# Performance work log

Hardware: AMD Instinct MI355X
Metric: run time of the kernel (lower is better)

Reference implementation:

```python
import jax, jax.numpy as jnp
import numpy as np

NOPEN = 64
NNIN = 16
NUM_OUTPUT = 64
NLAYER = 4
H = 0.1
TF = 1.0
N_NODES = 50000
N_EDGES = 1600000


def setup_inputs() -> dict:
    key = jax.random.key(0)
    k1, k2, k3, k4, k5, k6 = jax.random.split(key, 6)
    xn = jax.random.normal(k1, (1, NNIN, N_NODES), dtype=jnp.float32)
    iInd = jax.random.randint(k2, (N_EDGES,), 0, N_NODES)
    jInd = jax.random.randint(k3, (N_EDGES,), 0, N_NODES)
    # learned parameters per original init
    K1Nopen = jax.random.normal(k4, (NOPEN, NNIN), dtype=jnp.float32) * 0.01
    KN1 = jnp.eye(NOPEN, dtype=jnp.float32) + jax.random.uniform(k5, (NOPEN, NOPEN), dtype=jnp.float32) * 0.001
    KNclose = jax.random.normal(k6, (NUM_OUTPUT, NOPEN), dtype=jnp.float32) * 0.01
    return {"xn": xn, "iInd": iInd, "jInd": jInd, "n_nodes": N_NODES,
            "K1Nopen": K1Nopen, "KN1": KN1, "KNclose": KNclose}


def _gcn_norm(I, J, n_nodes, dtype):
    # add self-loops, symmetric normalization deg^{-1/2}[row]*deg^{-1/2}[col]
    loops = jnp.arange(n_nodes, dtype=I.dtype)
    I2 = jnp.concatenate([I, loops])
    J2 = jnp.concatenate([J, loops])
    ew = jnp.ones(I2.shape[0], dtype=dtype)
    deg = jax.ops.segment_sum(ew, J2, num_segments=n_nodes)
    dinv = jnp.where(deg > 0, 1.0 / jnp.sqrt(deg), 0.0)
    w = dinv[I2] * dinv[J2]
    return I2, J2, w


def reference(xn, iInd, jInd, n_nodes, K1Nopen, KN1, KNclose):
    I, J, w = _gcn_norm(iInd, jInd, n_nodes, xn.dtype)  # [E+N]

    # OpenFlatLayer: 1x1 conv1d with K1Nopen + relu (openclose=True, norm=False)
    x = jax.nn.relu(jnp.einsum('oi,bin->bon', K1Nopen, xn))  # [1, nopen, N]

    dt = TF / NLAYER
    wb = w[None, None, :]
    for _ in range(NLAYER):
        # nodeGrad: edge features [1, nopen, E]
        g = wb * (x[:, :, I] - x[:, :, J])
        # singleLayer (openclose=False): conv(K), relu, conv(K.t())
        z = jax.nn.relu(jnp.einsum('oi,bie->boe', KN1, g))
        z = jnp.einsum('io,bie->boe', KN1, z)
        # edgeDiv: scatter-add w*z at I minus at J
        wz = jnp.moveaxis(wb * z, -1, 0)  # [E, 1, nopen]
        div = (jax.ops.segment_sum(wz, I, num_segments=n_nodes)
               - jax.ops.segment_sum(wz, J, num_segments=n_nodes))
        div = jnp.moveaxis(div, 0, -1)  # [1, nopen, N]
        # forward Euler: step layer returns -h*div, integrated with dt
        x = x - dt * H * div

    # CloseLayer: 1x1 conv1d, squeeze().t(), log_softmax over channels
    xc = jnp.einsum('oi,bin->bon', KNclose, x)[0].T  # [N, num_output]
    return jax.nn.log_softmax(xc, axis=1)
```

## Files before the change

kernel.cpp:

```cpp
#include <hip/hip_runtime.h>

#define NN 50000
#define NE 1600000
#define C 64
#define NIN 16
#define DTH 0.025f
#define ASC 16.0f
#define USC 64.0f
#define SDIV 16384.0f
#define SLOT 128

#define NB2 256
#define NPB 196
#define CAP 16384
#define ABLK 1024
#define EPB 1563
#define RND 2048
#define BINC 32
#define GSTR 16

typedef _Float16 f16x2 __attribute__((ext_vector_type(2)));
typedef float f32x2 __attribute__((ext_vector_type(2)));
union U32H2 { uint32_t u; f16x2 h; };

#define RL(x, l) __int_as_float(__builtin_amdgcn_readlane(__float_as_int(x), (l)))

__global__ void k_setup(const float* __restrict__ KN1, const float* __restrict__ KNc,
                        float* __restrict__ M2s, float* __restrict__ KMs,
                        int* __restrict__ gcur) {
    if (threadIdx.x < NB2) gcur[threadIdx.x * GSTR] = 0;
    for (int idx = threadIdx.x; idx < C * C; idx += blockDim.x) {
        int p = idx >> 6, o = idx & 63;
        float s1 = 0.f, s2 = 0.f;
        for (int i = 0; i < C; i++) {
            s1 = fmaf(KN1[o * C + i], KN1[p * C + i], s1);
            s2 = fmaf(KNc[o * C + i], KN1[p * C + i], s2);
        }
        M2s[idx] = s1;
        KMs[idx] = s2;
    }
}

static __device__ __forceinline__ void store_u8(uint32_t* __restrict__ u8, int n, int lane, float su) {
    float v1 = __shfl_down(su, 1, 64);
    float v2 = __shfl_down(su, 2, 64);
    float v3 = __shfl_down(su, 3, 64);
    if ((lane & 3) == 0) {
        int p0 = __builtin_amdgcn_cvt_pk_fp8_f32(su, v1, 0, false);
        int p1 = __builtin_amdgcn_cvt_pk_fp8_f32(v2, v3, p0, true);
        u8[n * 16 + (lane >> 2)] = (uint32_t)p1;
    }
}

__launch_bounds__(512)
__global__ void k_binA_open(const int* __restrict__ iInd, const int* __restrict__ jInd,
                            int* __restrict__ gcur, uint32_t* __restrict__ stg,
                            const float* __restrict__ xn, const float* __restrict__ K1,
                            const float* __restrict__ KN1, const float* __restrict__ KNc,
                            _Float16* __restrict__ u0, uint32_t* __restrict__ u8,
                            float* __restrict__ co) {
    __shared__ __align__(16) char smem[36864];
    __shared__ int bcnt[NB2];
    __shared__ int gbase[NB2];
    __shared__ float sxn[NIN][17];
    uint32_t (*bins)[BINC] = (uint32_t(*)[BINC])smem;
    int tid = threadIdx.x;
    int eBeg = blockIdx.x * EPB;
    int eEnd = eBeg + EPB; if (eEnd > NE) eEnd = NE;
    for (int rb = eBeg; rb < eEnd; rb += RND) {
        for (int b = tid; b < NB2; b += 512) bcnt[b] = 0;
        __syncthreads();
        int rEnd = rb + RND; if (rEnd > eEnd) rEnd = eEnd;
        for (int e = rb + tid; e < rEnd; e += 512) {
            int i = __builtin_nontemporal_load(&iInd[e]);
            int j = __builtin_nontemporal_load(&jInd[e]);
            {
                int b = (unsigned)i / NPB;
                uint32_t ent = ((unsigned)(i - b * NPB) << 17) | (unsigned)j;
                int pos = atomicAdd(&bcnt[b], 1);
                if (pos < BINC) bins[b][pos] = ent;
                else { int gp = atomicAdd(&gcur[b * GSTR], 1);
                       if (gp < CAP) stg[(size_t)b * CAP + gp] = ent; }
            }
            {
                int b = (unsigned)j / NPB;
                uint32_t ent = ((unsigned)(j - b * NPB) << 17) | 0x10000u | (unsigned)i;
                int pos = atomicAdd(&bcnt[b], 1);
                if (pos < BINC) bins[b][pos] = ent;
                else { int gp = atomicAdd(&gcur[b * GSTR], 1);
                       if (gp < CAP) stg[(size_t)b * CAP + gp] = ent; }
            }
        }
        __syncthreads();
        if (tid < NB2) {
            int c = bcnt[tid]; if (c > BINC) c = BINC;
            gbase[tid] = (c > 0) ? atomicAdd(&gcur[tid * GSTR], c) : 0;
        }
        __syncthreads();
        for (int idx = tid; idx < NB2 * BINC; idx += 512) {
            int b = idx >> 5, k = idx & (BINC - 1);
            int c = bcnt[b]; if (c > BINC) c = BINC;
            if (k < c) {
                int pos = gbase[b] + k;
                if (pos < CAP) stg[(size_t)b * CAP + pos] = bins[b][k];
            }
        }
        __syncthreads();
    }
    float* sK1 = (float*)smem;
    float* sU  = sK1 + NIN * C;
    float* sC  = sU + C * C;
    for (int idx = tid; idx < NIN * C; idx += 512) {
        int i = idx >> 6, o = idx & 63;
        sK1[idx] = K1[o * NIN + i];
    }
    for (int idx = tid; idx < C * C; idx += 512) {
        int o = idx >> 6, p = idx & 63;
        int sw = (o << 6) | (p ^ ((o & 7) << 2));
        sU[sw] = KN1[idx];
        sC[sw] = KNc[idx];
    }
    int wv = tid >> 6, lane = tid & 63;
    int mb = lane << 6, lx = (lane & 7) << 2;
    int w2 = wv * 2;
    int nit = 3 + (blockIdx.x < 53 ? 1 : 0);
    int fi = tid >> 4, ft = tid & 15;
    float vpre = 0.f;
    if (tid < 256) vpre = xn[fi * NN + blockIdx.x * 16 + ft];
    for (int it = 0; it < nit; it++) {
        __syncthreads();
        if (tid < 256) sxn[fi][ft] = vpre;
        __syncthreads();
        if (it + 1 < nit && tid < 256)
            vpre = xn[fi * NN + blockIdx.x * 16 + (it + 1) * 16384 + ft];
        int pr = blockIdx.x * 8 + wv + it * 8192;
        int nA = pr * 2, nB = nA + 1;
        float xA = 0.f, xB = 0.f;
#pragma unroll
        for (int i = 0; i < NIN; i++) {
            float k1 = sK1[i * C + lane];
            xA = fmaf(k1, sxn[i][w2], xA);
            xB = fmaf(k1, sxn[i][w2 + 1], xB);
        }
        xA = fmaxf(xA, 0.f); xB = fmaxf(xB, 0.f);
        float uA0 = 0.f, uA1 = 0.f, uB0 = 0.f, uB1 = 0.f;
        float cA0 = 0.f, cA1 = 0.f, cB0 = 0.f, cB1 = 0.f;
#pragma unroll
        for (int p0 = 0; p0 < C; p0 += 4) {
            const float4 mu = *(const float4*)&sU[mb + (p0 ^ lx)];
            const float4 mc = *(const float4*)&sC[mb + (p0 ^ lx)];
            float a0 = RL(xA, p0 + 0), a1 = RL(xA, p0 + 1);
            float a2 = RL(xA, p0 + 2), a3 = RL(xA, p0 + 3);
            float b0 = RL(xB, p0 + 0), b1 = RL(xB, p0 + 1);
            float b2 = RL(xB, p0 + 2), b3 = RL(xB, p0 + 3);
            uA0 = fmaf(mu.x, a0, uA0); uA1 = fmaf(mu.y, a1, uA1);
            uA0 = fmaf(mu.z, a2, uA0); uA1 = fmaf(mu.w, a3, uA1);
            uB0 = fmaf(mu.x, b0, uB0); uB1 = fmaf(mu.y, b1, uB1);
            uB0 = fmaf(mu.z, b2, uB0); uB1 = fmaf(mu.w, b3, uB1);
            cA0 = fmaf(mc.x, a0, cA0); cA1 = fmaf(mc.y, a1, cA1);
            cA0 = fmaf(mc.z, a2, cA0); cA1 = fmaf(mc.w, a3, cA1);
            cB0 = fmaf(mc.x, b0, cB0); cB1 = fmaf(mc.y, b1, cB1);
            cB0 = fmaf(mc.z, b2, cB0); cB1 = fmaf(mc.w, b3, cB1);
        }
        float uA = uA0 + uA1, uB = uB0 + uB1;
        u0[(size_t)nA * C + lane] = (_Float16)uA;
        u0[(size_t)nB * C + lane] = (_Float16)uB;
        store_u8(u8, nA, lane, uA * USC);
        store_u8(u8, nB, lane, uB * USC);
        co[(size_t)nA * C + lane] = cA0 + cA1;
        co[(size_t)nB * C + lane] = cB0 + cB1;
    }
}

#define LADJ (NPB * SLOT)
__launch_bounds__(1024)
__global__ void k_binB(const int* __restrict__ gcur, const uint32_t* __restrict__ stg,
                       unsigned* __restrict__ pk, float* __restrict__ dinv,
                       uint32_t* __restrict__ adjp) {
    __shared__ unsigned lcnt[NPB];
    __shared__ uint32_t ladj[LADJ];
    int b = blockIdx.x, tid = threadIdx.x;
    if (tid < NPB) lcnt[tid] = 0;
    __syncthreads();
    int cnt = gcur[b * GSTR]; if (cnt > CAP) cnt = CAP;
    int n0 = b * NPB;
    for (int k = tid; k < cnt; k += 1024) {
        uint32_t ent = stg[(size_t)b * CAP + k];
        int tl = (int)(ent >> 17);
        unsigned sign = (ent >> 16) & 1u;
        unsigned other = ent & 0xFFFFu;
        unsigned ret = atomicAdd(&lcnt[tl], 1u + (sign << 16));
        unsigned slot = ret & 0xFFFFu;
        if (slot < SLOT) ladj[(tl << 7) + slot] = other | (sign << 31);
    }
    __syncthreads();
    if (tid < NPB) {
        int n = n0 + tid;
        if (n < NN) {
            unsigned v = lcnt[tid];
            unsigned c = v & 0xFFFFu; if (c > SLOT) c = SLOT;
            unsigned deg = (v >> 16) + 1u;
            pk[n] = (deg << 16) | c;
            dinv[n] = 1.0f / sqrtf((float)deg);
        }
    }
    int nval = NN - n0; if (nval > NPB) nval = NPB; if (nval < 0) nval = 0;
    int totv = (nval << 7) >> 2;
    uint4* gdst = (uint4*)(adjp + ((size_t)n0 << 7));
    const uint4* lsrc = (const uint4*)ladj;
    for (int v = tid; v < totv; v += 1024) gdst[v] = lsrc[v];
}

__global__ void k_weight(const unsigned* __restrict__ pk, const float* __restrict__ dinv,
                         uint32_t* __restrict__ adjp) {
    int idx = blockIdx.x * 256 + threadIdx.x;
    int n = idx >> 7, p = idx & (SLOT - 1);
    int cnt = (int)(pk[n] & 0xFFFFu); if (cnt > SLOT) cnt = SLOT;
    int pad = (cnt + 31) & ~31;
    if (p < cnt) {
        uint32_t e = adjp[idx];
        int other = (int)(e & 0xFFFFu);
        float a = ASC * dinv[n] * dinv[other];
        float w = 0.5f * a * a;
        if (e >> 31) w = -w;
        U32H2 t; t.u = (unsigned)other; t.h.y = (_Float16)w;
        adjp[idx] = t.u;
    } else if (p < pad) {
        adjp[idx] = 0u;
    }
}

#define ACCR(WW, QQ, A0, A1, A2, A3, U0, U1, U2, U3) {                        \
    U32H2 aw; aw.u = (WW);                                                    \
    float w_ = (float)aw.h.y;                                                 \
    f32x2 lo_ = __builtin_amdgcn_cvt_pk_f32_fp8((int)(QQ), false);            \
    f32x2 hi_ = __builtin_amdgcn_cvt_pk_f32_fp8((int)(QQ), true);             \
    float d0_ = (U0) - lo_.x, d1_ = (U1) - lo_.y;                             \
    float d2_ = (U2) - hi_.x, d3_ = (U3) - hi_.y;                             \
    A0 = fmaf(w_, __builtin_fabsf(d0_), fmaf(__builtin_fabsf(w_), d0_, A0));  \
    A1 = fmaf(w_, __builtin_fabsf(d1_), fmaf(__builtin_fabsf(w_), d1_, A1));  \
    A2 = fmaf(w_, __builtin_fabsf(d2_), fmaf(__builtin_fabsf(w_), d2_, A2));  \
    A3 = fmaf(w_, __builtin_fabsf(d3_), fmaf(__builtin_fabsf(w_), d3_, A3));  \
}

#define GATHER2_BODY(PKA, ADJP, U8R)                                          \
    uint32_t unqA = (U8R)[nA * 16 + li];                                      \
    uint32_t unqB = (U8R)[nB * 16 + li];                                      \
    f32x2 alo = __builtin_amdgcn_cvt_pk_f32_fp8((int)unqA, false);            \
    f32x2 ahi = __builtin_amdgcn_cvt_pk_f32_fp8((int)unqA, true);             \
    f32x2 blo = __builtin_amdgcn_cvt_pk_f32_fp8((int)unqB, false);            \
    f32x2 bhi = __builtin_amdgcn_cvt_pk_f32_fp8((int)unqB, true);             \
    float uA0 = alo.x, uA1 = alo.y, uA2 = ahi.x, uA3 = ahi.y;                 \
    float uB0 = blo.x, uB1 = blo.y, uB2 = bhi.x, uB3 = bhi.y;                 \
    uint2 pk2_ = *(const uint2*)&(PKA)[nA];                                   \
    int degA = (int)(pk2_.x & 0xFFFFu); if (degA > SLOT) degA = SLOT;         \
    int degB = (int)(pk2_.y & 0xFFFFu); if (degB > SLOT) degB = SLOT;         \
    int padA = (degA + 31) & ~31, padB = (degB + 31) & ~31;                   \
    int baseA = nA << 7, baseB = nB << 7;                                     \
    int maxPad = padA > padB ? padA : padB;                                   \
    float aA0 = 0.f, aA1 = 0.f, aA2 = 0.f, aA3 = 0.f;                         \
    float aB0 = 0.f, aB1 = 0.f, aB2 = 0.f, aB3 = 0.f;                         \
    for (int c0 = 0; c0 < maxPad; c0 += 32) {                                 \
        uint32_t wA[8], qA[8], wB[8], qB[8];                                  \
        bool dA = c0 < padA, dB = c0 < padB;                                  \
        if (dA) {                                                             \
            _Pragma("unroll")                                                 \
            for (int r = 0; r < 8; r++) wA[r] = (ADJP)[baseA + c0 + r * 4 + g]; \
        }                                                                     \
        if (dB) {                                                             \
            _Pragma("unroll")                                                 \
            for (int r = 0; r < 8; r++) wB[r] = (ADJP)[baseB + c0 + r * 4 + g]; \
        }                                                                     \
        if (dA) {                                                             \
            _Pragma("unroll")                                                 \
            for (int r = 0; r < 8; r++) qA[r] = (U8R)[(wA[r] & 0xFFFFu) * 16 + li]; \
        }                                                                     \
        if (dB) {                                                             \
            _Pragma("unroll")                                                 \
            for (int r = 0; r < 8; r++) qB[r] = (U8R)[(wB[r] & 0xFFFFu) * 16 + li]; \
        }                                                                     \
        if (dA) {                                                             \
            _Pragma("unroll")                                                 \
            for (int r = 0; r < 8; r++) ACCR(wA[r], qA[r], aA0, aA1, aA2, aA3, uA0, uA1, uA2, uA3) \
        }                                                                     \
        if (dB) {                                                             \
            _Pragma("unroll")                                                 \
            for (int r = 0; r < 8; r++) ACCR(wB[r], qB[r], aB0, aB1, aB2, aB3, uB0, uB1, uB2, uB3) \
        }                                                                     \
    }                                                                         \
    aA0 += __shfl_xor(aA0, 16, 64); aA0 += __shfl_xor(aA0, 32, 64);           \
    aA1 += __shfl_xor(aA1, 16, 64); aA1 += __shfl_xor(aA1, 32, 64);           \
    aA2 += __shfl_xor(aA2, 16, 64); aA2 += __shfl_xor(aA2, 32, 64);           \
    aA3 += __shfl_xor(aA3, 16, 64); aA3 += __shfl_xor(aA3, 32, 64);           \
    aB0 += __shfl_xor(aB0, 16, 64); aB0 += __shfl_xor(aB0, 32, 64);           \
    aB1 += __shfl_xor(aB1, 16, 64); aB1 += __shfl_xor(aB1, 32, 64);           \
    aB2 += __shfl_xor(aB2, 16, 64); aB2 += __shfl_xor(aB2, 32, 64);           \
    aB3 += __shfl_xor(aB3, 16, 64); aB3 += __shfl_xor(aB3, 32, 64);           \
    float rA0 = __shfl(aA0, lane >> 2, 64), rA1 = __shfl(aA1, lane >> 2, 64); \
    float rA2 = __shfl(aA2, lane >> 2, 64), rA3 = __shfl(aA3, lane >> 2, 64); \
    float rB0 = __shfl(aB0, lane >> 2, 64), rB1 = __shfl(aB1, lane >> 2, 64); \
    float rB2 = __shfl(aB2, lane >> 2, 64), rB3 = __shfl(aB3, lane >> 2, 64); \
    float sA_lane = (lane & 2) ? ((lane & 1) ? rA3 : rA2)                     \
                               : ((lane & 1) ? rA1 : rA0);                    \
    float sB_lane = (lane & 2) ? ((lane & 1) ? rB3 : rB2)                     \
                               : ((lane & 1) ? rB1 : rB0);

#define STAGE_MT(SMT, SRC) {                                                  \
    for (int idx = threadIdx.x; idx < C * C; idx += 256) {                    \
        int p_ = idx >> 6, c_ = idx & 63;                                     \
        (SMT)[(c_ << 6) | (p_ ^ ((c_ & 7) << 2))] = (SRC)[idx];               \
    }                                                                         \
}

#define MATVEC2(SMT, SAV, SBV, DUA, DUB) {                                    \
    float mA0_ = 0.f, mA1_ = 0.f, mB0_ = 0.f, mB1_ = 0.f;                     \
    int mb_ = (lane << 6), lx_ = (lane & 7) << 2;                             \
    _Pragma("unroll")                                                         \
    for (int p0 = 0; p0 < 64; p0 += 4) {                                      \
        const float4 mv = *(const float4*)&(SMT)[mb_ + (p0 ^ lx_)];           \
        mA0_ = fmaf(mv.x, RL(SAV, p0 + 0), mA0_);                             \
        mA1_ = fmaf(mv.y, RL(SAV, p0 + 1), mA1_);                             \
        mA0_ = fmaf(mv.z, RL(SAV, p0 + 2), mA0_);                             \
        mA1_ = fmaf(mv.w, RL(SAV, p0 + 3), mA1_);                             \
        mB0_ = fmaf(mv.x, RL(SBV, p0 + 0), mB0_);                             \
        mB1_ = fmaf(mv.y, RL(SBV, p0 + 1), mB1_);                             \
        mB0_ = fmaf(mv.z, RL(SBV, p0 + 2), mB0_);                             \
        mB1_ = fmaf(mv.w, RL(SBV, p0 + 3), mB1_);                             \
    }                                                                         \
    DUA = mA0_ + mA1_; DUB = mB0_ + mB1_;                                     \
}

__launch_bounds__(256, 8)
__global__ void k_gather_upd(const unsigned* __restrict__ pk, const uint32_t* __restrict__ adjp,
                             const uint32_t* __restrict__ u8r, const _Float16* __restrict__ ucur,
                             const float* __restrict__ M2s, float* __restrict__ sacc,
                             _Float16* __restrict__ unext, uint32_t* __restrict__ u8w, int beta) {
    __shared__ float sMt[C * C];
    STAGE_MT(sMt, M2s)
    __syncthreads();
    int wv = threadIdx.x >> 6, lane = threadIdx.x & 63;
    int g = lane >> 4, li = lane & 15;
    int nA = (blockIdx.x * 4 + wv) * 2;
    int nB = nA + 1;
    GATHER2_BODY(pk, adjp, u8r)
    float duA, duB;
    MATVEC2(sMt, sA_lane, sB_lane, duA, duB)
    float unewA = (float)ucur[(size_t)nA * C + lane] - (DTH / SDIV) * duA;
    float unewB = (float)ucur[(size_t)nB * C + lane] - (DTH / SDIV) * duB;
    unext[(size_t)nA * C + lane] = (_Float16)unewA;
    unext[(size_t)nB * C + lane] = (_Float16)unewB;
    store_u8(u8w, nA, lane, unewA * USC);
    store_u8(u8w, nB, lane, unewB * USC);
    size_t ixA = (size_t)nA * C + lane, ixB = (size_t)nB * C + lane;
    sacc[ixA] = beta ? (sacc[ixA] + sA_lane) : sA_lane;
    sacc[ixB] = beta ? (sacc[ixB] + sB_lane) : sB_lane;
}

__launch_bounds__(256, 8)
__global__ void k_gather_close(const unsigned* __restrict__ pk, const uint32_t* __restrict__ adjp,
                               const uint32_t* __restrict__ u8r, const float* __restrict__ KMs,
                               const float* __restrict__ sacc, const float* __restrict__ co,
                               float* __restrict__ out) {
    __shared__ float sKMt[C * C];
    STAGE_MT(sKMt, KMs)
    __syncthreads();
    int wv = threadIdx.x >> 6, lane = threadIdx.x & 63;
    int g = lane >> 4, li = lane & 15;
    int nA = (blockIdx.x * 4 + wv) * 2;
    int nB = nA + 1;
    GATHER2_BODY(pk, adjp, u8r)
    float stotA = sA_lane + sacc[(size_t)nA * C + lane];
    float stotB = sB_lane + sacc[(size_t)nB * C + lane];
    float dxA, dxB;
    MATVEC2(sKMt, stotA, stotB, dxA, dxB)
    float oA = co[(size_t)nA * C + lane] - (DTH / SDIV) * dxA;
    float oB = co[(size_t)nB * C + lane] - (DTH / SDIV) * dxB;
    float mA = oA, mB = oB;
#pragma unroll
    for (int off2 = 32; off2; off2 >>= 1) {
        mA = fmaxf(mA, __shfl_xor(mA, off2, 64));
        mB = fmaxf(mB, __shfl_xor(mB, off2, 64));
    }
    float sumA = expf(oA - mA), sumB = expf(oB - mB);
#pragma unroll
    for (int off2 = 32; off2; off2 >>= 1) {
        sumA += __shfl_xor(sumA, off2, 64);
        sumB += __shfl_xor(sumB, off2, 64);
    }
    out[(size_t)nA * C + lane] = oA - mA - logf(sumA);
    out[(size_t)nB * C + lane] = oB - mB - logf(sumB);
}

extern "C" void kernel_launch(void* const* d_in, const int* in_sizes, int n_in,
                              void* d_out, int out_size, void* d_ws, size_t ws_size,
                              hipStream_t stream) {
    (void)in_sizes; (void)n_in; (void)out_size; (void)ws_size;
    const float* xn   = (const float*)d_in[0];
    const int* iInd   = (const int*)d_in[1];
    const int* jInd   = (const int*)d_in[2];
    const float* K1   = (const float*)d_in[4];
    const float* KN1  = (const float*)d_in[5];
    const float* KNc  = (const float*)d_in[6];
    float* out = (float*)d_out;

    char* base = (char*)d_ws;
    size_t off = 0;
    auto alloc = [&](size_t bytes) { char* p = base + off; off = (off + bytes + 255) & ~(size_t)255; return p; };
    float* M2s  = (float*)alloc(C * C * 4);
    float* KMs  = (float*)alloc(C * C * 4);
    int* gcur   = (int*)alloc(NB2 * GSTR * 4);
    unsigned* pk = (unsigned*)alloc(NN * 4);
    float* dinv = (float*)alloc(NN * 4);
    float* co   = (float*)alloc((size_t)NN * C * 4);
    float* sacc = (float*)alloc((size_t)NN * C * 4);
    _Float16* ua = (_Float16*)alloc((size_t)NN * C * 2);
    _Float16* ub = (_Float16*)alloc((size_t)NN * C * 2);
    uint32_t* u8a = (uint32_t*)alloc((size_t)NN * 16 * 4);
    uint32_t* u8b = (uint32_t*)alloc((size_t)NN * 16 * 4);
    uint32_t* stg = (uint32_t*)alloc((size_t)NB2 * CAP * 4);
    uint32_t* adjp = (uint32_t*)alloc((size_t)NN * SLOT * 4);

    k_setup<<<1, 256, 0, stream>>>(KN1, KNc, M2s, KMs, gcur);
    k_binA_open<<<ABLK, 512, 0, stream>>>(iInd, jInd, gcur, stg, xn, K1, KN1, KNc, ua, u8a, co);
    k_binB<<<NB2, 1024, 0, stream>>>(gcur, stg, pk, dinv, adjp);
    k_weight<<<(NN * SLOT) / 256, 256, 0, stream>>>(pk, dinv, adjp);

    const int GB = NN / 8;
    k_gather_upd<<<GB, 256, 0, stream>>>(pk, adjp, u8a, ua, M2s, sacc, ub, u8b, 0);
    k_gather_upd<<<GB, 256, 0, stream>>>(pk, adjp, u8b, ub, M2s, sacc, ua, u8a, 1);
    k_gather_upd<<<GB, 256, 0, stream>>>(pk, adjp, u8a, ua, M2s, sacc, ub, u8b, 1);
    k_gather_close<<<GB, 256, 0, stream>>>(pk, adjp, u8b, KMs, sacc, co, out);
}
```

Before: 459.6 us.

## Prefetch next adjacency chunk, pack accumulation math, store raw edge weight

```diff
diff --git a/kernel.cpp b/kernel.cpp
--- a/kernel.cpp
+++ b/kernel.cpp
@@ -221,73 +221,91 @@
         uint32_t e = adjp[idx];
         int other = (int)(e & 0xFFFFu);
         float a = ASC * dinv[n] * dinv[other];
-        float w = 0.5f * a * a;
-        if (e >> 31) w = -w;
-        U32H2 t; t.u = (unsigned)other; t.h.y = (_Float16)w;
+        if (e >> 31) a = -a;
+        U32H2 t; t.u = (unsigned)other; t.h.y = (_Float16)a;
         adjp[idx] = t.u;
     } else if (p < pad) {
         adjp[idx] = 0u;
     }
 }
 
-#define ACCR(WW, QQ, A0, A1, A2, A3, U0, U1, U2, U3) {                        \
+#define ACCR(WW, QQ, A01, A23, U01, U23) {                                    \
     U32H2 aw; aw.u = (WW);                                                    \
-    float w_ = (float)aw.h.y;                                                 \
+    float a_ = (float)aw.h.y;                                                 \
+    f32x2 av_; av_.x = a_; av_.y = a_;                                        \
     f32x2 lo_ = __builtin_amdgcn_cvt_pk_f32_fp8((int)(QQ), false);            \
     f32x2 hi_ = __builtin_amdgcn_cvt_pk_f32_fp8((int)(QQ), true);             \
-    float d0_ = (U0) - lo_.x, d1_ = (U1) - lo_.y;                             \
-    float d2_ = (U2) - hi_.x, d3_ = (U3) - hi_.y;                             \
-    A0 = fmaf(w_, __builtin_fabsf(d0_), fmaf(__builtin_fabsf(w_), d0_, A0));  \
-    A1 = fmaf(w_, __builtin_fabsf(d1_), fmaf(__builtin_fabsf(w_), d1_, A1));  \
-    A2 = fmaf(w_, __builtin_fabsf(d2_), fmaf(__builtin_fabsf(w_), d2_, A2));  \
-    A3 = fmaf(w_, __builtin_fabsf(d3_), fmaf(__builtin_fabsf(w_), d3_, A3));  \
+    f32x2 t01_ = av_ * ((U01) - lo_);                                         \
+    f32x2 t23_ = av_ * ((U23) - hi_);                                         \
+    t01_ = __builtin_elementwise_max(t01_, zz);                               \
+    t23_ = __builtin_elementwise_max(t23_, zz);                               \
+    A01 = av_ * t01_ + A01;                                                   \
+    A23 = av_ * t23_ + A23;                                                   \
 }
 
 #define GATHER2_BODY(PKA, ADJP, U8R)                                          \
     uint32_t unqA = (U8R)[nA * 16 + li];                                      \
     uint32_t unqB = (U8R)[nB * 16 + li];                                      \
-    f32x2 alo = __builtin_amdgcn_cvt_pk_f32_fp8((int)unqA, false);            \
-    f32x2 ahi = __builtin_amdgcn_cvt_pk_f32_fp8((int)unqA, true);             \
-    f32x2 blo = __builtin_amdgcn_cvt_pk_f32_fp8((int)unqB, false);            \
-    f32x2 bhi = __builtin_amdgcn_cvt_pk_f32_fp8((int)unqB, true);             \
-    float uA0 = alo.x, uA1 = alo.y, uA2 = ahi.x, uA3 = ahi.y;                 \
-    float uB0 = blo.x, uB1 = blo.y, uB2 = bhi.x, uB3 = bhi.y;                 \
+    f32x2 uA01 = __builtin_amdgcn_cvt_pk_f32_fp8((int)unqA, false);           \
+    f32x2 uA23 = __builtin_amdgcn_cvt_pk_f32_fp8((int)unqA, true);            \
+    f32x2 uB01 = __builtin_amdgcn_cvt_pk_f32_fp8((int)unqB, false);           \
+    f32x2 uB23 = __builtin_amdgcn_cvt_pk_f32_fp8((int)unqB, true);            \
     uint2 pk2_ = *(const uint2*)&(PKA)[nA];                                   \
     int degA = (int)(pk2_.x & 0xFFFFu); if (degA > SLOT) degA = SLOT;         \
     int degB = (int)(pk2_.y & 0xFFFFu); if (degB > SLOT) degB = SLOT;         \
     int padA = (degA + 31) & ~31, padB = (degB + 31) & ~31;                   \
     int baseA = nA << 7, baseB = nB << 7;                                     \
     int maxPad = padA > padB ? padA : padB;                                   \
-    float aA0 = 0.f, aA1 = 0.f, aA2 = 0.f, aA3 = 0.f;                         \
-    float aB0 = 0.f, aB1 = 0.f, aB2 = 0.f, aB3 = 0.f;                         \
+    f32x2 zz; zz.x = 0.f; zz.y = 0.f;                                         \
+    f32x2 aA01 = zz, aA23 = zz, aB01 = zz, aB23 = zz;                         \
+    uint32_t wA[8], wB[8];                                                    \
+    if (padA > 0) {                                                           \
+        _Pragma("unroll")                                                     \
+        for (int r = 0; r < 8; r++) wA[r] = (ADJP)[baseA + r * 4 + g];        \
+    }                                                                         \
+    if (padB > 0) {                                                           \
+        _Pragma("unroll")                                                     \
+        for (int r = 0; r < 8; r++) wB[r] = (ADJP)[baseB + r * 4 + g];        \
+    }                                                                         \
     for (int c0 = 0; c0 < maxPad; c0 += 32) {                                 \
-        uint32_t wA[8], qA[8], wB[8], qB[8];                                  \
+        uint32_t qA[8], qB[8], wA2[8], wB2[8];                                \
         bool dA = c0 < padA, dB = c0 < padB;                                  \
+        bool dA2 = c0 + 32 < padA, dB2 = c0 + 32 < padB;                      \
         if (dA) {                                                             \
             _Pragma("unroll")                                                 \
-            for (int r = 0; r < 8; r++) wA[r] = (ADJP)[baseA + c0 + r * 4 + g]; \
+            for (int r = 0; r < 8; r++) qA[r] = (U8R)[(wA[r] & 0xFFFFu) * 16 + li]; \
         }                                                                     \
         if (dB) {                                                             \
             _Pragma("unroll")                                                 \
-            for (int r = 0; r < 8; r++) wB[r] = (ADJP)[baseB + c0 + r * 4 + g]; \
+            for (int r = 0; r < 8; r++) qB[r] = (U8R)[(wB[r] & 0xFFFFu) * 16 + li]; \
+        }                                                                     \
+        if (dA2) {                                                            \
+            _Pragma("unroll")                                                 \
+            for (int r = 0; r < 8; r++) wA2[r] = (ADJP)[baseA + c0 + 32 + r * 4 + g]; \
+        }                                                                     \
+        if (dB2) {                                                            \
+            _Pragma("unroll")                                                 \
+            for (int r = 0; r < 8; r++) wB2[r] = (ADJP)[baseB + c0 + 32 + r * 4 + g]; \
         }                                                                     \
         if (dA) {                                                             \
             _Pragma("unroll")                                                 \
-            for (int r = 0; r < 8; r++) qA[r] = (U8R)[(wA[r] & 0xFFFFu) * 16 + li]; \
+            for (int r = 0; r < 8; r++) ACCR(wA[r], qA[r], aA01, aA23, uA01, uA23) \
         }                                                                     \
         if (dB) {                                                             \
             _Pragma("unroll")                                                 \
-            for (int r = 0; r < 8; r++) qB[r] = (U8R)[(wB[r] & 0xFFFFu) * 16 + li]; \
-        }                                                                     \
-        if (dA) {                                                             \
-            _Pragma("unroll")                                                 \
-            for (int r = 0; r < 8; r++) ACCR(wA[r], qA[r], aA0, aA1, aA2, aA3, uA0, uA1, uA2, uA3) \
-        }                                                                     \
-        if (dB) {                                                             \
-            _Pragma("unroll")                                                 \
-            for (int r = 0; r < 8; r++) ACCR(wB[r], qB[r], aB0, aB1, aB2, aB3, uB0, uB1, uB2, uB3) \
+            for (int r = 0; r < 8; r++) ACCR(wB[r], qB[r], aB01, aB23, uB01, uB23) \
+        }                                                                     \
+        if (dA2) {                                                            \
+            _Pragma("unroll")                                                 \
+            for (int r = 0; r < 8; r++) wA[r] = wA2[r];                       \
+        }                                                                     \
+        if (dB2) {                                                            \
+            _Pragma("unroll")                                                 \
+            for (int r = 0; r < 8; r++) wB[r] = wB2[r];                       \
         }                                                                     \
     }                                                                         \
+    float aA0 = aA01.x, aA1 = aA01.y, aA2 = aA23.x, aA3 = aA23.y;             \
+    float aB0 = aB01.x, aB1 = aB01.y, aB2 = aB23.x, aB3 = aB23.y;             \
     aA0 += __shfl_xor(aA0, 16, 64); aA0 += __shfl_xor(aA0, 32, 64);           \
     aA1 += __shfl_xor(aA1, 16, 64); aA1 += __shfl_xor(aA1, 32, 64);           \
     aA2 += __shfl_xor(aA2, 16, 64); aA2 += __shfl_xor(aA2, 32, 64);           \
@@ -330,7 +348,7 @@
     DUA = mA0_ + mA1_; DUB = mB0_ + mB1_;                                     \
 }
 
-__launch_bounds__(256, 8)
+__launch_bounds__(256, 6)
 __global__ void k_gather_upd(const unsigned* __restrict__ pk, const uint32_t* __restrict__ adjp,
                              const uint32_t* __restrict__ u8r, const _Float16* __restrict__ ucur,
                              const float* __restrict__ M2s, float* __restrict__ sacc,
@@ -356,7 +374,7 @@
     sacc[ixB] = beta ? (sacc[ixB] + sB_lane) : sB_lane;
 }
 
-__launch_bounds__(256, 8)
+__launch_bounds__(256, 6)
 __global__ void k_gather_close(const unsigned* __restrict__ pk, const uint32_t* __restrict__ adjp,
                                const uint32_t* __restrict__ u8r, const float* __restrict__ KMs,
                                const float* __restrict__ sacc, const float* __restrict__ co,
```

Result: no change. 460.7 us (+0.3%).
